# Kernel tuning notes

Hardware: AMD Instinct MI355X
Metric: run time of the kernel (lower is better)

Reference implementation:

```python
import jax, jax.numpy as jnp
import numpy as np

B, T, D = 2, 2048, 2048
H, HKV = 16, 16
SEM, GEO = 1024, 1024
DH = D // H          # 128, v head dim
DS = SEM // H        # 64, sem head dim
DG = GEO // H        # 64, geo head dim (== rope_dim)
ROPE_BASE = 10000.0


def _split_heads(x, n_heads, hd):
    b, t, _ = x.shape
    return x.reshape(b, t, n_heads, hd).transpose(0, 2, 1, 3)  # (B,H,T,hd)


def _rope(x, pos_offset):
    # x: (B,H,T,DG); rotate-half RoPE over the full geo head dim
    b, h, t, d = x.shape
    inv_freq = 1.0 / (ROPE_BASE ** (jnp.arange(0, d, 2, dtype=jnp.float32) / d))
    pos = jnp.arange(t, dtype=jnp.float32) + jnp.float32(pos_offset)
    ang = pos[:, None] * inv_freq[None, :]            # (T, d/2)
    cos, sin = jnp.cos(ang), jnp.sin(ang)             # (T, d/2)
    x1, x2 = x[..., : d // 2], x[..., d // 2 :]
    return jnp.concatenate([x1 * cos - x2 * sin, x2 * cos + x1 * sin], axis=-1)


def setup_inputs() -> dict:
    key = jax.random.key(0)
    ks = jax.random.split(key, 8)
    s = lambda fan_in: 1.0 / np.sqrt(fan_in)
    return {
        "x": jax.random.normal(ks[0], (B, T, D), dtype=jnp.float32),
        "Wq_sem": jax.random.normal(ks[1], (D, SEM), dtype=jnp.float32) * s(D),
        "Wk_sem": jax.random.normal(ks[2], (D, SEM), dtype=jnp.float32) * s(D),
        "Wq_geo": jax.random.normal(ks[3], (D, GEO), dtype=jnp.float32) * s(D),
        "Wk_geo": jax.random.normal(ks[4], (D, GEO), dtype=jnp.float32) * s(D),
        "Wv": jax.random.normal(ks[5], (D, D), dtype=jnp.float32) * s(D),
        "Wo": jax.random.normal(ks[6], (D, D), dtype=jnp.float32) * s(D),
        "gate_logit": jax.random.normal(ks[7], (H,), dtype=jnp.float32) * 0.1,
        "pos_offset": 0,
    }


def reference(x, Wq_sem, Wk_sem, Wq_geo, Wk_geo, Wv, Wo, gate_logit, pos_offset):
    qsh = _split_heads(x @ Wq_sem, H, DS)    # (B,H,T,DS)
    ksh = _split_heads(x @ Wk_sem, HKV, DS)
    qgh = _split_heads(x @ Wq_geo, H, DG)    # (B,H,T,DG)
    kgh = _split_heads(x @ Wk_geo, HKV, DG)
    vh = _split_heads(x @ Wv, HKV, DH)       # (B,H,T,DH)

    qgh = _rope(qgh, pos_offset)
    kgh = _rope(kgh, pos_offset)

    gate = jax.nn.sigmoid(gate_logit).reshape(1, H, 1, 1).astype(x.dtype)
    qsh = qsh * (2.0 * gate)
    qgh = qgh * (2.0 - 2.0 * gate)

    sem_scale = 1.0 / np.sqrt(float(DS))
    geo_scale = 1.0 / np.sqrt(float(DG))
    # decoupled logits: sem and geo contributions each with their own scale
    logits = (jnp.einsum("bhqd,bhkd->bhqk", qsh, ksh) * sem_scale
              + jnp.einsum("bhqd,bhkd->bhqk", qgh, kgh) * geo_scale)

    t = x.shape[1]
    causal = jnp.tril(jnp.ones((t, t), dtype=bool))
    logits = jnp.where(causal, logits, jnp.finfo(logits.dtype).min)
    attn = jax.nn.softmax(logits, axis=-1)

    out_h = jnp.einsum("bhqk,bhkd->bhqd", attn, vh)   # (B,H,T,DH)
    out = out_h.transpose(0, 2, 1, 3).reshape(x.shape[0], t, H * DH)
    return out @ Wo
```

## Files before the change

kernel.cpp:

```cpp
#include <hip/hip_runtime.h>
#include <hip/hip_bf16.h>
#include <math.h>

#define B_ 2
#define T_ 2048
#define D_ 2048
#define H_ 16
#define DH_ 128
#define SEM_ 1024
#define GEO_ 1024
#define NPROJ 6144

typedef unsigned short ushort_t;
typedef short bf16x8 __attribute__((ext_vector_type(8)));
typedef float f32x4 __attribute__((ext_vector_type(4)));
typedef unsigned short us4 __attribute__((ext_vector_type(4)));
typedef unsigned short us2 __attribute__((ext_vector_type(2)));

static __device__ inline ushort_t f2b(float x) {
    __hip_bfloat16 h = __float2bfloat16(x);
    return *reinterpret_cast<ushort_t*>(&h);
}
static __device__ inline float b2f(ushort_t u) {
    union { unsigned int i; float f; } v; v.i = ((unsigned int)u) << 16; return v.f;
}
static __device__ inline void gload_lds16(const ushort_t* g, ushort_t* l) {
    __builtin_amdgcn_global_load_lds(
        (const __attribute__((address_space(1))) void*)g,
        (__attribute__((address_space(3))) void*)l, 16, 0, 0);
}

#define BARS()  { asm volatile("" ::: "memory"); __builtin_amdgcn_s_barrier(); asm volatile("" ::: "memory"); }
#define WL0()   asm volatile("s_waitcnt lgkmcnt(0)" ::: "memory")
#define WV6()   asm volatile("s_waitcnt vmcnt(6)" ::: "memory")
#define WV4()   asm volatile("s_waitcnt vmcnt(4)" ::: "memory")
#define WV0()   asm volatile("s_waitcnt vmcnt(0)" ::: "memory")

__global__ __launch_bounds__(256) void convert_x(
    const float* __restrict__ x, ushort_t* __restrict__ xh)
{
    size_t i = ((size_t)blockIdx.x * 256 + threadIdx.x) * 8;
    float4 a = *(const float4*)&x[i];
    float4 b = *(const float4*)&x[i + 4];
    bf16x8 o;
    o[0] = (short)f2b(a.x); o[1] = (short)f2b(a.y);
    o[2] = (short)f2b(a.z); o[3] = (short)f2b(a.w);
    o[4] = (short)f2b(b.x); o[5] = (short)f2b(b.y);
    o[6] = (short)f2b(b.z); o[7] = (short)f2b(b.w);
    *(bf16x8*)&xh[i] = o;
}

__global__ __launch_bounds__(256) void transpose_all(
    const float* __restrict__ W0, const float* __restrict__ W1,
    const float* __restrict__ W2, const float* __restrict__ W3,
    const float* __restrict__ W4, const float* __restrict__ W5,
    ushort_t* __restrict__ Wt_all, ushort_t* __restrict__ WoT)
{
    const int z = blockIdx.z;
    const float* W;
    ushort_t* dst;
    int N;
    switch (z) {
        case 0: W = W0; dst = Wt_all;                          N = 1024; break;
        case 1: W = W1; dst = Wt_all + (size_t)1024 * 2048;    N = 1024; break;
        case 2: W = W2; dst = Wt_all + (size_t)2048 * 2048;    N = 1024; break;
        case 3: W = W3; dst = Wt_all + (size_t)3072 * 2048;    N = 1024; break;
        case 4: W = W4; dst = Wt_all + (size_t)4096 * 2048;    N = 2048; break;
        default: W = W5; dst = WoT;                            N = 2048; break;
    }
    const int n0 = blockIdx.x * 64;
    if (n0 >= N) return;
    const int k0 = blockIdx.y * 64;

    __shared__ float tile[64][66];
    const int c2 = (threadIdx.x & 31) * 2;
    const int r  = threadIdx.x >> 5;
#pragma unroll
    for (int rr = 0; rr < 64; rr += 8) {
        float2 v = *(const float2*)&W[(size_t)(k0 + r + rr) * N + n0 + c2];
        tile[r + rr][c2]     = v.x;
        tile[r + rr][c2 + 1] = v.y;
    }
    __syncthreads();
    const int kc = (threadIdx.x & 31) * 2;
#pragma unroll
    for (int rr = 0; rr < 64; rr += 8) {
        int nrow = r + rr;
        us2 o;
        o[0] = f2b(tile[kc][nrow]);
        o[1] = f2b(tile[kc + 1][nrow]);
        *(us2*)&dst[(size_t)(n0 + nrow) * 2048 + k0 + kc] = o;
    }
}

#define LDA8(par, iq, i4, kk) \
    (*(const bf16x8*)&smA[(par)*16384 + (iq)*8192 + aoff + (i4)*1024 + ((kk) ? ca1 : ca0)])
#define LDB8(par, jq, j1, kk) \
    (*(const bf16x8*)&smB[(par)*16384 + (jq)*8192 + boff + (j1)*2048 + ((kk) ? ca1 : ca0)])

#define READ_A(par, iq) \
    aF[0]=LDA8(par,iq,0,0); aF[1]=LDA8(par,iq,0,1); \
    aF[2]=LDA8(par,iq,1,0); aF[3]=LDA8(par,iq,1,1); \
    aF[4]=LDA8(par,iq,2,0); aF[5]=LDA8(par,iq,2,1); \
    aF[6]=LDA8(par,iq,3,0); aF[7]=LDA8(par,iq,3,1);

#define READ_B(par, jq) \
    bF[(jq)*4+0]=LDB8(par,jq,0,0); bF[(jq)*4+1]=LDB8(par,jq,0,1); \
    bF[(jq)*4+2]=LDB8(par,jq,1,0); bF[(jq)*4+3]=LDB8(par,jq,1,1);

#define STAGE_A(h, kt, par) do { \
    const ushort_t* _s = gAbase + (size_t)((h)*128) * 2048 + (kt)*64 + stgoff; \
    ushort_t* _d = smA + (par)*16384 + (h)*8192 + wid*512; \
    gload_lds16(_s, _d); \
    gload_lds16(_s + (size_t)64*2048, _d + 4096); \
} while(0)

#define STAGE_B(h, kt, par) do { \
    const ushort_t* _s = gBbase + (size_t)((h)*128) * 2048 + (kt)*64 + stgoff; \
    ushort_t* _d = smB + (par)*16384 + (h)*8192 + wid*512; \
    gload_lds16(_s, _d); \
    gload_lds16(_s + (size_t)64*2048, _d + 4096); \
} while(0)

#define MM16(iq, jq) do { \
    _Pragma("unroll") \
    for (int i4 = 0; i4 < 4; ++i4) { \
        acc[(iq)*4+i4][(jq)*2+0] = __builtin_amdgcn_mfma_f32_16x16x32_bf16(aF[i4*2+0], bF[(jq)*4+0], acc[(iq)*4+i4][(jq)*2+0], 0, 0, 0); \
        acc[(iq)*4+i4][(jq)*2+0] = __builtin_amdgcn_mfma_f32_16x16x32_bf16(aF[i4*2+1], bF[(jq)*4+1], acc[(iq)*4+i4][(jq)*2+0], 0, 0, 0); \
        acc[(iq)*4+i4][(jq)*2+1] = __builtin_amdgcn_mfma_f32_16x16x32_bf16(aF[i4*2+0], bF[(jq)*4+2], acc[(iq)*4+i4][(jq)*2+1], 0, 0, 0); \
        acc[(iq)*4+i4][(jq)*2+1] = __builtin_amdgcn_mfma_f32_16x16x32_bf16(aF[i4*2+1], bF[(jq)*4+3], acc[(iq)*4+i4][(jq)*2+1], 0, 0, 0); \
    } \
} while(0)

#define TILE_BODY(par, parn, kt1, kt2) \
    STAGE_A(1, kt1, parn); \
    BARS(); WL0(); \
    __builtin_amdgcn_s_setprio(1); MM16(0, 0); __builtin_amdgcn_s_setprio(0); \
    READ_B(par, 1); \
    BARS(); \
    STAGE_A(0, kt2, par); \
    BARS(); WL0(); \
    __builtin_amdgcn_s_setprio(1); MM16(0, 1); __builtin_amdgcn_s_setprio(0); \
    READ_A(par, 1); \
    BARS(); \
    STAGE_B(0, kt2, par); \
    BARS(); WL0(); \
    __builtin_amdgcn_s_setprio(1); MM16(1, 1); __builtin_amdgcn_s_setprio(0); \
    BARS(); \
    STAGE_B(1, kt2, par); WV6(); \
    BARS(); \
    __builtin_amdgcn_s_setprio(1); MM16(1, 0); __builtin_amdgcn_s_setprio(0); \
    READ_A(parn, 0); READ_B(parn, 0); \
    BARS();

__global__ __launch_bounds__(512, 2) void gemm_proj(
    const ushort_t* __restrict__ A, const ushort_t* __restrict__ Bt,
    const float* __restrict__ gate_logit, const int* __restrict__ pos_off,
    ushort_t* __restrict__ Qh, ushort_t* __restrict__ Kh,
    ushort_t* __restrict__ Vt)
{
    extern __shared__ __align__(16) ushort_t smdyn[];
    ushort_t* smA = smdyn;
    ushort_t* smB = smdyn + 32768;

    const int tid  = threadIdx.x;
    const int wid  = tid >> 6, lane = tid & 63;
    const int ln16 = lane & 15, g = lane >> 4;
    const int wm = wid & 1, wn = wid >> 1;
    const int m0 = blockIdx.y * 256, n0 = blockIdx.x * 256;

    const int srow = wid * 8 + (lane >> 3);
    const int scol = ((lane & 7) ^ (lane >> 3)) * 8;
    const size_t stgoff = (size_t)srow * 2048 + scol;
    const ushort_t* gAbase = A  + (size_t)m0 * 2048;
    const ushort_t* gBbase = Bt + (size_t)n0 * 2048;

    const int cg0 = ln16 & 7;
    const int ca0 = ((g + 0) ^ cg0) * 8;
    const int ca1 = ((g + 4) ^ cg0) * 8;
    const int aoff = wm * 4096 + ln16 * 64;
    const int boff = (wn >> 1) * 4096 + (wn & 1) * 1024 + ln16 * 64;

    f32x4 acc[8][4];
#pragma unroll
    for (int i = 0; i < 8; ++i)
#pragma unroll
        for (int j = 0; j < 4; ++j) acc[i][j] = (f32x4){0.f, 0.f, 0.f, 0.f};
    bf16x8 aF[8], bF[8];

    STAGE_A(0, 0, 0); STAGE_B(0, 0, 0); STAGE_B(1, 0, 0); STAGE_A(1, 0, 0);
    STAGE_A(0, 1, 1); STAGE_B(0, 1, 1); STAGE_B(1, 1, 1);
    WV6();
    BARS();
    READ_A(0, 0); READ_B(0, 0);

#pragma unroll 1
    for (int t = 0; t < 32; t += 2) {
        const int ka1 = t + 1;
        const int ka2 = (t + 2 < 32) ? t + 2 : 31;
        const int kb1 = ka2;
        const int kb2 = (t + 3 < 32) ? t + 3 : 31;
        TILE_BODY(0, 1, ka1, ka2);
        TILE_BODY(1, 0, kb1, kb2);
    }
    asm volatile("s_waitcnt vmcnt(0) lgkmcnt(0)" ::: "memory");

    const int region = n0 >> 10;
    const int rbase  = m0 + wm * 64 + g * 4;

    if (region <= 1) {
        ushort_t* dst = (region == 0) ? Qh : Kh;
        const int hb  = ((n0 & 1023) >> 6) + (wn >> 1);
        const int d64 = (wn & 1) * 16 + ln16;
        float sc0 = 1.0f, sc1 = 1.0f;
        if (region == 0) {
            sc0 = 0.25f / (1.0f + __expf(-gate_logit[hb]));
            sc1 = 0.25f / (1.0f + __expf(-gate_logit[hb + 2]));
        }
#pragma unroll
        for (int i = 0; i < 8; ++i)
#pragma unroll
            for (int r = 0; r < 4; ++r) {
                int row = rbase + (i >> 2) * 128 + (i & 3) * 16 + r;
                int t = row & (T_ - 1), bb = row >> 11;
                size_t b0 = ((size_t)(bb * H_ + hb)     * T_ + t) * 128;
                size_t b1 = ((size_t)(bb * H_ + hb + 2) * T_ + t) * 128;
                dst[b0 + d64]      = f2b(acc[i][0][r] * sc0);
                dst[b0 + d64 + 32] = f2b(acc[i][1][r] * sc0);
                dst[b1 + d64]      = f2b(acc[i][2][r] * sc1);
                dst[b1 + d64 + 32] = f2b(acc[i][3][r] * sc1);
            }
    } else if (region <= 3) {
        ushort_t* dst = (region == 2) ? Qh : Kh;
        const int hb = ((n0 & 1023) >> 6) + (wn >> 1);
        const int ip = (wn & 1) * 16 + ln16;
        const float invf = __expf(-0.28782313665087625f * (float)ip);
        const float po = (float)(*pos_off);
        float sc0 = 1.0f, sc1 = 1.0f;
        if (region == 2) {
            sc0 = 0.25f * (1.0f - 1.0f / (1.0f + __expf(-gate_logit[hb])));
            sc1 = 0.25f * (1.0f - 1.0f / (1.0f + __expf(-gate_logit[hb + 2])));
        }
#pragma unroll
        for (int i = 0; i < 8; ++i)
#pragma unroll
            for (int r = 0; r < 4; ++r) {
                int row = rbase + (i >> 2) * 128 + (i & 3) * 16 + r;
                int t = row & (T_ - 1), bb = row >> 11;
                float s, c;
                __sincosf(((float)t + po) * invf, &s, &c);
                size_t b0 = ((size_t)(bb * H_ + hb)     * T_ + t) * 128;
                size_t b1 = ((size_t)(bb * H_ + hb + 2) * T_ + t) * 128;
                float x1 = acc[i][0][r], x2 = acc[i][1][r];
                dst[b0 + 64 + ip] = f2b((x1 * c - x2 * s) * sc0);
                dst[b0 + 96 + ip] = f2b((x2 * c + x1 * s) * sc0);
                x1 = acc[i][2][r]; x2 = acc[i][3][r];
                dst[b1 + 64 + ip] = f2b((x1 * c - x2 * s) * sc1);
                dst[b1 + 96 + ip] = f2b((x2 * c + x1 * s) * sc1);
            }
    } else {
        const int hb = (n0 - 4096) >> 7;
        const int db = (wn >> 1) * 64 + (wn & 1) * 16 + ln16;
#pragma unroll
        for (int i = 0; i < 8; ++i) {
            int row0 = rbase + (i >> 2) * 128 + (i & 3) * 16;
            int t0 = row0 & (T_ - 1), bb = row0 >> 11;
#pragma unroll
            for (int j = 0; j < 4; ++j) {
                us4 v;
                v[0] = f2b(acc[i][j][0]); v[1] = f2b(acc[i][j][1]);
                v[2] = f2b(acc[i][j][2]); v[3] = f2b(acc[i][j][3]);
                int hh = hb + (j >> 1);
                int dd = db + (j & 1) * 32;
                *(us4*)&Vt[((size_t)(bb * H_ + hh) * DH_ + dd) * T_ + t0] = v;
            }
        }
    }
}

#define BT_STAGE(k, buf) do { \
    gload_lds16(gA + (k),       As + (buf)*4096 + wid*1024); \
    gload_lds16(gA + (k) + K16, As + (buf)*4096 + wid*1024 + 512); \
    gload_lds16(gB + (k),       Bs + (buf)*4096 + wid*1024); \
    gload_lds16(gB + (k) + K16, Bs + (buf)*4096 + wid*1024 + 512); \
} while(0)

__global__ __launch_bounds__(256) void gemm_bt_f32(
    const ushort_t* __restrict__ A, const ushort_t* __restrict__ Bt,
    float* __restrict__ C, int M, int N, int K)
{
    __shared__ ushort_t As[2 * 128 * 32];
    __shared__ ushort_t Bs[2 * 128 * 32];

    const int tid  = threadIdx.x;
    const int wid  = tid >> 6, lane = tid & 63;
    const int ln16 = lane & 15, g = lane >> 4;
    const int wm = wid & 1, wn = wid >> 1;
    const int m0 = blockIdx.y * 128, n0 = blockIdx.x * 128;

    const int lrow = lane >> 2;
    const int lc8  = (lane & 3) * 8;
    const ushort_t* gA = A  + (size_t)(m0 + wid * 32 + lrow) * K + lc8;
    const ushort_t* gB = Bt + (size_t)(n0 + wid * 32 + lrow) * K + lc8;
    const size_t K16 = (size_t)16 * K;

    f32x4 acc[4][4];
#pragma unroll
    for (int i = 0; i < 4; ++i)
#pragma unroll
        for (int j = 0; j < 4; ++j) acc[i][j] = (f32x4){0.f, 0.f, 0.f, 0.f};

    const int nk = K >> 5;
    BT_STAGE(0, 0);
    BT_STAGE(32, 1);

#pragma unroll 1
    for (int kb = 0; kb < nk; ++kb) {
        if (kb + 1 < nk) { WV4(); } else { WV0(); }
        BARS();

        const int bufo = (kb & 1) * 4096;
        bf16x8 af[4], bfr[4];
#pragma unroll
        for (int i = 0; i < 4; ++i)
            af[i] = *(const bf16x8*)&As[bufo + (wm * 64 + i * 16 + ln16) * 32 + g * 8];
#pragma unroll
        for (int j = 0; j < 4; ++j)
            bfr[j] = *(const bf16x8*)&Bs[bufo + (wn * 64 + j * 16 + ln16) * 32 + g * 8];
        __builtin_amdgcn_s_setprio(1);
#pragma unroll
        for (int i = 0; i < 4; ++i)
#pragma unroll
            for (int j = 0; j < 4; ++j)
                acc[i][j] = __builtin_amdgcn_mfma_f32_16x16x32_bf16(
                    af[i], bfr[j], acc[i][j], 0, 0, 0);
        __builtin_amdgcn_s_setprio(0);
        WL0();
        BARS();

        if (kb + 2 < nk) BT_STAGE((size_t)(kb + 2) * 32, kb & 1);
    }

#pragma unroll
    for (int i = 0; i < 4; ++i)
#pragma unroll
        for (int j = 0; j < 4; ++j)
#pragma unroll
            for (int r = 0; r < 4; ++r) {
                int row = m0 + wm * 64 + i * 16 + g * 4 + r;
                int col = n0 + wn * 64 + j * 16 + ln16;
                C[(size_t)row * N + col] = acc[i][j][r];
            }
}

#define P_PITCH  40

#define FA_STAGE(kt, buf) do { \
    gload_lds16(Kbase + (size_t)((kt) + kr0) * 128 + kofs0, Ks + (buf)*4096 + wid * 512); \
    gload_lds16(Kbase + (size_t)((kt) + kr1) * 128 + kofs1, Ks + (buf)*4096 + 2048 + wid * 512); \
    gload_lds16(Vbase + (size_t)vd0 * T_ + (kt) + vofs0,    Vs + (buf)*4096 + wid * 512); \
    gload_lds16(Vbase + (size_t)vd1 * T_ + (kt) + vofs1,    Vs + (buf)*4096 + 2048 + wid * 512); \
} while(0)

__global__ __launch_bounds__(256) void flash_attn(
    const ushort_t* __restrict__ Qh,
    const ushort_t* __restrict__ Kh,
    const ushort_t* __restrict__ Vt,
    ushort_t* __restrict__ aoh)
{
    __shared__ ushort_t Ks[2 * 32 * 128];
    __shared__ ushort_t Vs[2 * 128 * 32];
    __shared__ ushort_t Pl[4 * 16 * P_PITCH];

    const int tid  = threadIdx.x;
    const int wid  = tid >> 6, lane = tid & 63;
    const int ln16 = lane & 15, g = lane >> 4;

    const int lin = blockIdx.x + (blockIdx.y << 4) + (blockIdx.z << 8);
    const int h = lin & 15;
    const int b = (lin >> 4) & 1;
    const int p = lin >> 5;
    const int bh = b * H_ + h;

    const ushort_t* Kbase = Kh + (size_t)bh * T_ * 128;
    const ushort_t* Vbase = Vt + (size_t)bh * 128 * T_;
    ushort_t* Pw = Pl + wid * 16 * P_PITCH;

    const int sk0 = tid,      sk1 = 256 + tid;
    const int kr0 = sk0 >> 4, kc0 = sk0 & 15;
    const int kr1 = sk1 >> 4, kc1 = sk1 & 15;
    const int vd0 = sk0 >> 2, vg0 = sk0 & 3;
    const int vd1 = sk1 >> 2, vg1 = sk1 & 3;
    const int kofs0 = (kc0 ^ (kr0 & 15)) * 8, kofs1 = (kc1 ^ (kr1 & 15)) * 8;
    const int vofs0 = (vg0 ^ ((vd0 + (vd0 >> 2)) & 3)) * 8;
    const int vofs1 = (vg1 ^ ((vd1 + (vd1 >> 2)) & 3)) * 8;

    bf16x8 bones;
    {
        short o = (ln16 == 0) ? (short)0x3F80 : (short)0;
#pragma unroll
        for (int j = 0; j < 8; ++j) bones[j] = o;
    }

#pragma unroll 1
    for (int ti = 0; ti < 2; ++ti) {
        const int qt = ti ? (31 - p) : p;
        const int q0 = qt * 64;
        const int qw = q0 + wid * 16;

        bf16x8 aq[4];
        {
            const ushort_t* qrow = Qh + ((size_t)bh * T_ + qw + ln16) * 128;
#pragma unroll
            for (int c2 = 0; c2 < 4; ++c2)
                aq[c2] = *(const bf16x8*)(qrow + c2 * 32 + g * 8);
        }

        f32x4 acc[8];
#pragma unroll
        for (int i = 0; i < 8; ++i) acc[i] = (f32x4){0.f, 0.f, 0.f, 0.f};
        f32x4 acc_l = (f32x4){0.f, 0.f, 0.f, 0.f};

        const int nkb  = q0 / 32 + 2;
        const int qmax = qw + 15;

        FA_STAGE(0, 0);
        FA_STAGE(32, 1);

#pragma unroll 1
        for (int kb = 0; kb < nkb; ++kb) {
            const int kt = kb * 32;
            if (kb + 1 < nkb) { WV4(); } else { WV0(); }
            BARS();

            if (kt <= qmax) {
                const int kbuf = (kb & 1) * 4096;

                f32x4 s0 = (f32x4){0.f, 0.f, 0.f, 0.f};
                f32x4 s1 = (f32x4){0.f, 0.f, 0.f, 0.f};
                __builtin_amdgcn_s_setprio(1);
#pragma unroll
                for (int c2 = 0; c2 < 4; ++c2) {
                    int jk = c2 * 4 + g;
                    bf16x8 bk0 = *(const bf16x8*)&Ks[kbuf + (ln16 * 16 + (jk ^ ln16)) * 8];
                    bf16x8 bk1 = *(const bf16x8*)&Ks[kbuf + (256 + ln16 * 16 + (jk ^ ln16)) * 8];
                    s0 = __builtin_amdgcn_mfma_f32_16x16x32_bf16(aq[c2], bk0, s0, 0, 0, 0);
                    s1 = __builtin_amdgcn_mfma_f32_16x16x32_bf16(aq[c2], bk1, s1, 0, 0, 0);
                }
                __builtin_amdgcn_s_setprio(0);

                const bool diag = (kt + 31 > qw);
#pragma unroll
                for (int r2 = 0; r2 < 4; ++r2) {
                    float e0 = __expf(s0[r2] - 12.0f);
                    float e1 = __expf(s1[r2] - 12.0f);
                    if (diag) {
                        int qr = qw + g * 4 + r2;
                        e0 = (kt + ln16      > qr) ? 0.0f : e0;
                        e1 = (kt + 16 + ln16 > qr) ? 0.0f : e1;
                    }
                    int prow = g * 4 + r2;
                    Pw[prow * P_PITCH + ln16]      = f2b(e0);
                    Pw[prow * P_PITCH + 16 + ln16] = f2b(e1);
                }
                __asm__ volatile("s_waitcnt lgkmcnt(0)" ::: "memory");
                bf16x8 ap = *(const bf16x8*)&Pw[ln16 * P_PITCH + g * 8];

                __builtin_amdgcn_s_setprio(1);
#pragma unroll
                for (int cdv = 0; cdv < 8; ++cdv) {
                    int d = cdv * 16 + ln16;
                    bf16x8 bv = *(const bf16x8*)
                        &Vs[kbuf + ((d << 2) + (g ^ ((d + (d >> 2)) & 3))) * 8];
                    acc[cdv] = __builtin_amdgcn_mfma_f32_16x16x32_bf16(ap, bv, acc[cdv], 0, 0, 0);
                }
                acc_l = __builtin_amdgcn_mfma_f32_16x16x32_bf16(ap, bones, acc_l, 0, 0, 0);
                __builtin_amdgcn_s_setprio(0);
                WL0();
            }

            BARS();
            if (kb + 2 < nkb) FA_STAGE(kt + 64, kb & 1);
        }

        float invl[4];
#pragma unroll
        for (int r2 = 0; r2 < 4; ++r2)
            invl[r2] = 1.0f / __shfl(acc_l[r2], lane & 48);
#pragma unroll
        for (int cdv = 0; cdv < 8; ++cdv)
#pragma unroll
            for (int r2 = 0; r2 < 4; ++r2) {
                int qr = qw + g * 4 + r2;
                aoh[((size_t)b * T_ + qr) * D_ + h * DH_ + cdv * 16 + ln16] =
                    f2b(acc[cdv][r2] * invl[r2]);
            }
    }
}

extern "C" void kernel_launch(void* const* d_in, const int* in_sizes, int n_in,
                              void* d_out, int out_size, void* d_ws, size_t ws_size,
                              hipStream_t stream)
{
    const float* x       = (const float*)d_in[0];
    const float* Wq_sem  = (const float*)d_in[1];
    const float* Wk_sem  = (const float*)d_in[2];
    const float* Wq_geo  = (const float*)d_in[3];
    const float* Wk_geo  = (const float*)d_in[4];
    const float* Wv      = (const float*)d_in[5];
    const float* Wo      = (const float*)d_in[6];
    const float* gate    = (const float*)d_in[7];
    const int*   pos_off = (const int*)d_in[8];
    float* out = (float*)d_out;

    const int M = B_ * T_;
    char* ws = (char*)d_ws;
    ushort_t* xh     = (ushort_t*)(ws);
    ushort_t* aoh    = xh;
    ushort_t* Wt_all = (ushort_t*)(ws + (size_t)16 * 1048576);
    ushort_t* WoT    = (ushort_t*)(ws + (size_t)40 * 1048576);
    ushort_t* Qh     = (ushort_t*)(ws + (size_t)48 * 1048576);
    ushort_t* Kh     = (ushort_t*)(ws + (size_t)64 * 1048576);
    ushort_t* Vt     = (ushort_t*)(ws + (size_t)80 * 1048576);

    dim3 blk(256);

    convert_x<<<(M * D_) / (256 * 8), blk, 0, stream>>>(x, xh);
    transpose_all<<<dim3(32, 32, 6), blk, 0, stream>>>(
        Wq_sem, Wk_sem, Wq_geo, Wk_geo, Wv, Wo, Wt_all, WoT);

    hipFuncSetAttribute((const void*)gemm_proj,
                        hipFuncAttributeMaxDynamicSharedMemorySize, 131072);
    gemm_proj<<<dim3(NPROJ / 256, M / 256), dim3(512), 131072, stream>>>(
        xh, Wt_all, gate, pos_off, Qh, Kh, Vt);

    flash_attn<<<dim3(16, H_, B_), blk, 0, stream>>>(Qh, Kh, Vt, aoh);

    gemm_bt_f32<<<dim3(D_ / 128, M / 128), blk, 0, stream>>>(
        aoh, WoT, out, M, D_, D_);
}
```

Baseline: 372.8 us.

## Shrink projection GEMM tile to 128x256 with three-stage LDS pipeline

The projection GEMM tile goes from 256x256 to 128x256 per block, and the two-buffer, four-phase A/B half-tile schedule becomes a triple-buffered pipeline that prefetches two k-steps ahead. The smaller tile doubles the grid and halves the accumulator registers per thread, aimed at better wave occupancy and CU fill. The epilogue is remapped to the new warp-to-column layout, including the RoPE pairing. In exchange, LDS use rises to 144KB, which likely allows only one block per CU despite launch_bounds(512,2), and each block gets less operand reuse.

```diff
diff --git a/kernel.cpp b/kernel.cpp
--- a/kernel.cpp
+++ b/kernel.cpp
@@ -93,65 +93,42 @@
     }
 }
 
-#define LDA8(par, iq, i4, kk) \
-    (*(const bf16x8*)&smA[(par)*16384 + (iq)*8192 + aoff + (i4)*1024 + ((kk) ? ca1 : ca0)])
-#define LDB8(par, jq, j1, kk) \
-    (*(const bf16x8*)&smB[(par)*16384 + (jq)*8192 + boff + (j1)*2048 + ((kk) ? ca1 : ca0)])
-
-#define READ_A(par, iq) \
-    aF[0]=LDA8(par,iq,0,0); aF[1]=LDA8(par,iq,0,1); \
-    aF[2]=LDA8(par,iq,1,0); aF[3]=LDA8(par,iq,1,1); \
-    aF[4]=LDA8(par,iq,2,0); aF[5]=LDA8(par,iq,2,1); \
-    aF[6]=LDA8(par,iq,3,0); aF[7]=LDA8(par,iq,3,1);
-
-#define READ_B(par, jq) \
-    bF[(jq)*4+0]=LDB8(par,jq,0,0); bF[(jq)*4+1]=LDB8(par,jq,0,1); \
-    bF[(jq)*4+2]=LDB8(par,jq,1,0); bF[(jq)*4+3]=LDB8(par,jq,1,1);
-
-#define STAGE_A(h, kt, par) do { \
-    const ushort_t* _s = gAbase + (size_t)((h)*128) * 2048 + (kt)*64 + stgoff; \
-    ushort_t* _d = smA + (par)*16384 + (h)*8192 + wid*512; \
+#define PLDA(par, i4, kk) \
+    (*(const bf16x8*)&smA[(par)*8192 + aoff + (i4)*1024 + ((kk) ? ca1 : ca0)])
+#define PLDB(par, j, kk) \
+    (*(const bf16x8*)&smB[(par)*16384 + boff + (j)*1024 + ((kk) ? ca1 : ca0)])
+
+#define PREAD_SET(par, kk, off) \
+    aF[(off)+0]=PLDA(par,0,kk); aF[(off)+1]=PLDA(par,1,kk); \
+    aF[(off)+2]=PLDA(par,2,kk); aF[(off)+3]=PLDA(par,3,kk); \
+    bF[(off)+0]=PLDB(par,0,kk); bF[(off)+1]=PLDB(par,1,kk); \
+    bF[(off)+2]=PLDB(par,2,kk); bF[(off)+3]=PLDB(par,3,kk);
+
+#define PMM(off) do { \
+    _Pragma("unroll") \
+    for (int i = 0; i < 4; ++i) { \
+        acc[i][0] = __builtin_amdgcn_mfma_f32_16x16x32_bf16(aF[(off)+i], bF[(off)+0], acc[i][0], 0, 0, 0); \
+        acc[i][1] = __builtin_amdgcn_mfma_f32_16x16x32_bf16(aF[(off)+i], bF[(off)+1], acc[i][1], 0, 0, 0); \
+        acc[i][2] = __builtin_amdgcn_mfma_f32_16x16x32_bf16(aF[(off)+i], bF[(off)+2], acc[i][2], 0, 0, 0); \
+        acc[i][3] = __builtin_amdgcn_mfma_f32_16x16x32_bf16(aF[(off)+i], bF[(off)+3], acc[i][3], 0, 0, 0); \
+    } \
+} while(0)
+
+#define PSTAGE_A(kt, par) do { \
+    const ushort_t* _s = gAbase + (size_t)(kt) * 64 + stgoff; \
+    ushort_t* _d = smA + (par)*8192 + wid*512; \
     gload_lds16(_s, _d); \
     gload_lds16(_s + (size_t)64*2048, _d + 4096); \
 } while(0)
 
-#define STAGE_B(h, kt, par) do { \
-    const ushort_t* _s = gBbase + (size_t)((h)*128) * 2048 + (kt)*64 + stgoff; \
-    ushort_t* _d = smB + (par)*16384 + (h)*8192 + wid*512; \
+#define PSTAGE_B(kt, par) do { \
+    const ushort_t* _s = gBbase + (size_t)(kt) * 64 + stgoff; \
+    ushort_t* _d = smB + (par)*16384 + wid*512; \
     gload_lds16(_s, _d); \
-    gload_lds16(_s + (size_t)64*2048, _d + 4096); \
+    gload_lds16(_s + (size_t)64*2048,  _d + 4096); \
+    gload_lds16(_s + (size_t)128*2048, _d + 8192); \
+    gload_lds16(_s + (size_t)192*2048, _d + 12288); \
 } while(0)
-
-#define MM16(iq, jq) do { \
-    _Pragma("unroll") \
-    for (int i4 = 0; i4 < 4; ++i4) { \
-        acc[(iq)*4+i4][(jq)*2+0] = __builtin_amdgcn_mfma_f32_16x16x32_bf16(aF[i4*2+0], bF[(jq)*4+0], acc[(iq)*4+i4][(jq)*2+0], 0, 0, 0); \
-        acc[(iq)*4+i4][(jq)*2+0] = __builtin_amdgcn_mfma_f32_16x16x32_bf16(aF[i4*2+1], bF[(jq)*4+1], acc[(iq)*4+i4][(jq)*2+0], 0, 0, 0); \
-        acc[(iq)*4+i4][(jq)*2+1] = __builtin_amdgcn_mfma_f32_16x16x32_bf16(aF[i4*2+0], bF[(jq)*4+2], acc[(iq)*4+i4][(jq)*2+1], 0, 0, 0); \
-        acc[(iq)*4+i4][(jq)*2+1] = __builtin_amdgcn_mfma_f32_16x16x32_bf16(aF[i4*2+1], bF[(jq)*4+3], acc[(iq)*4+i4][(jq)*2+1], 0, 0, 0); \
-    } \
-} while(0)
-
-#define TILE_BODY(par, parn, kt1, kt2) \
-    STAGE_A(1, kt1, parn); \
-    BARS(); WL0(); \
-    __builtin_amdgcn_s_setprio(1); MM16(0, 0); __builtin_amdgcn_s_setprio(0); \
-    READ_B(par, 1); \
-    BARS(); \
-    STAGE_A(0, kt2, par); \
-    BARS(); WL0(); \
-    __builtin_amdgcn_s_setprio(1); MM16(0, 1); __builtin_amdgcn_s_setprio(0); \
-    READ_A(par, 1); \
-    BARS(); \
-    STAGE_B(0, kt2, par); \
-    BARS(); WL0(); \
-    __builtin_amdgcn_s_setprio(1); MM16(1, 1); __builtin_amdgcn_s_setprio(0); \
-    BARS(); \
-    STAGE_B(1, kt2, par); WV6(); \
-    BARS(); \
-    __builtin_amdgcn_s_setprio(1); MM16(1, 0); __builtin_amdgcn_s_setprio(0); \
-    READ_A(parn, 0); READ_B(parn, 0); \
-    BARS();
 
 __global__ __launch_bounds__(512, 2) void gemm_proj(
     const ushort_t* __restrict__ A, const ushort_t* __restrict__ Bt,
@@ -161,13 +138,13 @@
 {
     extern __shared__ __align__(16) ushort_t smdyn[];
     ushort_t* smA = smdyn;
-    ushort_t* smB = smdyn + 32768;
+    ushort_t* smB = smdyn + 24576;
 
     const int tid  = threadIdx.x;
     const int wid  = tid >> 6, lane = tid & 63;
     const int ln16 = lane & 15, g = lane >> 4;
     const int wm = wid & 1, wn = wid >> 1;
-    const int m0 = blockIdx.y * 256, n0 = blockIdx.x * 256;
+    const int m0 = blockIdx.y * 128, n0 = blockIdx.x * 256;
 
     const int srow = wid * 8 + (lane >> 3);
     const int scol = ((lane & 7) ^ (lane >> 3)) * 8;
@@ -179,29 +156,36 @@
     const int ca0 = ((g + 0) ^ cg0) * 8;
     const int ca1 = ((g + 4) ^ cg0) * 8;
     const int aoff = wm * 4096 + ln16 * 64;
-    const int boff = (wn >> 1) * 4096 + (wn & 1) * 1024 + ln16 * 64;
-
-    f32x4 acc[8][4];
-#pragma unroll
-    for (int i = 0; i < 8; ++i)
+    const int boff = wn * 4096 + ln16 * 64;
+
+    f32x4 acc[4][4];
+#pragma unroll
+    for (int i = 0; i < 4; ++i)
 #pragma unroll
         for (int j = 0; j < 4; ++j) acc[i][j] = (f32x4){0.f, 0.f, 0.f, 0.f};
     bf16x8 aF[8], bF[8];
 
-    STAGE_A(0, 0, 0); STAGE_B(0, 0, 0); STAGE_B(1, 0, 0); STAGE_A(1, 0, 0);
-    STAGE_A(0, 1, 1); STAGE_B(0, 1, 1); STAGE_B(1, 1, 1);
+    PSTAGE_A(0, 0); PSTAGE_B(0, 0);
+    PSTAGE_A(1, 1); PSTAGE_B(1, 1);
     WV6();
     BARS();
-    READ_A(0, 0); READ_B(0, 0);
-
+    PREAD_SET(0, 0, 0);
+
+    int par = 0, pn1 = 1, pn2 = 2;
 #pragma unroll 1
-    for (int t = 0; t < 32; t += 2) {
-        const int ka1 = t + 1;
-        const int ka2 = (t + 2 < 32) ? t + 2 : 31;
-        const int kb1 = ka2;
-        const int kb2 = (t + 3 < 32) ? t + 3 : 31;
-        TILE_BODY(0, 1, ka1, ka2);
-        TILE_BODY(1, 0, kb1, kb2);
+    for (int t = 0; t < 32; ++t) {
+        const int t2 = t + 2;
+        if (t2 < 32) { PSTAGE_A(t2, pn2); PSTAGE_B(t2, pn2); }
+        BARS(); WL0();
+        __builtin_amdgcn_s_setprio(1); PMM(0); __builtin_amdgcn_s_setprio(0);
+        PREAD_SET(par, 1, 4);
+        BARS();
+        if (t < 30) { WV6(); } else { WV0(); }
+        BARS(); WL0();
+        __builtin_amdgcn_s_setprio(1); PMM(4); __builtin_amdgcn_s_setprio(0);
+        PREAD_SET(pn1, 0, 0);
+        BARS();
+        int tmp = par; par = pn1; pn1 = pn2; pn2 = tmp;
     }
     asm volatile("s_waitcnt vmcnt(0) lgkmcnt(0)" ::: "memory");
 
@@ -210,68 +194,59 @@
 
     if (region <= 1) {
         ushort_t* dst = (region == 0) ? Qh : Kh;
-        const int hb  = ((n0 & 1023) >> 6) + (wn >> 1);
-        const int d64 = (wn & 1) * 16 + ln16;
-        float sc0 = 1.0f, sc1 = 1.0f;
-        if (region == 0) {
-            sc0 = 0.25f / (1.0f + __expf(-gate_logit[hb]));
-            sc1 = 0.25f / (1.0f + __expf(-gate_logit[hb + 2]));
-        }
-#pragma unroll
-        for (int i = 0; i < 8; ++i)
+        const int hb = ((n0 & 1023) >> 6) + wn;
+        float sc = 1.0f;
+        if (region == 0) sc = 0.25f / (1.0f + __expf(-gate_logit[hb]));
+#pragma unroll
+        for (int i = 0; i < 4; ++i)
 #pragma unroll
             for (int r = 0; r < 4; ++r) {
-                int row = rbase + (i >> 2) * 128 + (i & 3) * 16 + r;
+                int row = rbase + i * 16 + r;
                 int t = row & (T_ - 1), bb = row >> 11;
-                size_t b0 = ((size_t)(bb * H_ + hb)     * T_ + t) * 128;
-                size_t b1 = ((size_t)(bb * H_ + hb + 2) * T_ + t) * 128;
-                dst[b0 + d64]      = f2b(acc[i][0][r] * sc0);
-                dst[b0 + d64 + 32] = f2b(acc[i][1][r] * sc0);
-                dst[b1 + d64]      = f2b(acc[i][2][r] * sc1);
-                dst[b1 + d64 + 32] = f2b(acc[i][3][r] * sc1);
+                size_t base = ((size_t)(bb * H_ + hb) * T_ + t) * 128;
+#pragma unroll
+                for (int j = 0; j < 4; ++j)
+                    dst[base + j * 16 + ln16] = f2b(acc[i][j][r] * sc);
             }
     } else if (region <= 3) {
         ushort_t* dst = (region == 2) ? Qh : Kh;
-        const int hb = ((n0 & 1023) >> 6) + (wn >> 1);
-        const int ip = (wn & 1) * 16 + ln16;
-        const float invf = __expf(-0.28782313665087625f * (float)ip);
+        const int hb = ((n0 & 1023) >> 6) + wn;
         const float po = (float)(*pos_off);
-        float sc0 = 1.0f, sc1 = 1.0f;
-        if (region == 2) {
-            sc0 = 0.25f * (1.0f - 1.0f / (1.0f + __expf(-gate_logit[hb])));
-            sc1 = 0.25f * (1.0f - 1.0f / (1.0f + __expf(-gate_logit[hb + 2])));
-        }
-#pragma unroll
-        for (int i = 0; i < 8; ++i)
+        const float invf0 = __expf(-0.28782313665087625f * (float)ln16);
+        const float invf1 = __expf(-0.28782313665087625f * (float)(16 + ln16));
+        float sc = 1.0f;
+        if (region == 2) sc = 0.25f * (1.0f - 1.0f / (1.0f + __expf(-gate_logit[hb])));
+#pragma unroll
+        for (int i = 0; i < 4; ++i)
 #pragma unroll
             for (int r = 0; r < 4; ++r) {
-                int row = rbase + (i >> 2) * 128 + (i & 3) * 16 + r;
+                int row = rbase + i * 16 + r;
                 int t = row & (T_ - 1), bb = row >> 11;
-                float s, c;
-                __sincosf(((float)t + po) * invf, &s, &c);
-                size_t b0 = ((size_t)(bb * H_ + hb)     * T_ + t) * 128;
-                size_t b1 = ((size_t)(bb * H_ + hb + 2) * T_ + t) * 128;
-                float x1 = acc[i][0][r], x2 = acc[i][1][r];
-                dst[b0 + 64 + ip] = f2b((x1 * c - x2 * s) * sc0);
-                dst[b0 + 96 + ip] = f2b((x2 * c + x1 * s) * sc0);
-                x1 = acc[i][2][r]; x2 = acc[i][3][r];
-                dst[b1 + 64 + ip] = f2b((x1 * c - x2 * s) * sc1);
-                dst[b1 + 96 + ip] = f2b((x2 * c + x1 * s) * sc1);
+                size_t base = ((size_t)(bb * H_ + hb) * T_ + t) * 128;
+                float s0, c0, s1, c1;
+                __sincosf(((float)t + po) * invf0, &s0, &c0);
+                __sincosf(((float)t + po) * invf1, &s1, &c1);
+                float x1 = acc[i][0][r], x2 = acc[i][2][r];
+                dst[base + 64 + ln16]      = f2b((x1 * c0 - x2 * s0) * sc);
+                dst[base + 96 + ln16]      = f2b((x2 * c0 + x1 * s0) * sc);
+                x1 = acc[i][1][r]; x2 = acc[i][3][r];
+                dst[base + 64 + 16 + ln16] = f2b((x1 * c1 - x2 * s1) * sc);
+                dst[base + 96 + 16 + ln16] = f2b((x2 * c1 + x1 * s1) * sc);
             }
     } else {
         const int hb = (n0 - 4096) >> 7;
-        const int db = (wn >> 1) * 64 + (wn & 1) * 16 + ln16;
-#pragma unroll
-        for (int i = 0; i < 8; ++i) {
-            int row0 = rbase + (i >> 2) * 128 + (i & 3) * 16;
+#pragma unroll
+        for (int i = 0; i < 4; ++i) {
+            int row0 = rbase + i * 16;
             int t0 = row0 & (T_ - 1), bb = row0 >> 11;
 #pragma unroll
             for (int j = 0; j < 4; ++j) {
+                int cb = wn * 64 + j * 16;
+                int hh = hb + (cb >> 7);
+                int dd = (cb & 127) + ln16;
                 us4 v;
                 v[0] = f2b(acc[i][j][0]); v[1] = f2b(acc[i][j][1]);
                 v[2] = f2b(acc[i][j][2]); v[3] = f2b(acc[i][j][3]);
-                int hh = hb + (j >> 1);
-                int dd = db + (j & 1) * 32;
                 *(us4*)&Vt[((size_t)(bb * H_ + hh) * DH_ + dd) * T_ + t0] = v;
             }
         }
@@ -530,8 +505,8 @@
         Wq_sem, Wk_sem, Wq_geo, Wk_geo, Wv, Wo, Wt_all, WoT);
 
     hipFuncSetAttribute((const void*)gemm_proj,
-                        hipFuncAttributeMaxDynamicSharedMemorySize, 131072);
-    gemm_proj<<<dim3(NPROJ / 256, M / 256), dim3(512), 131072, stream>>>(
+                        hipFuncAttributeMaxDynamicSharedMemorySize, 147456);
+    gemm_proj<<<dim3(NPROJ / 256, M / 128), dim3(512), 147456, stream>>>(
         xh, Wt_all, gate, pos_off, Qh, Kh, Vt);
 
     flash_attn<<<dim3(16, H_, B_), blk, 0, stream>>>(Qh, Kh, Vt, aoh);
```

Measured after the change: 380.5 us. +2.1%, slower.
